# Performance work log

Hardware: AMD Instinct MI355X
Metric: run time of the kernel (lower is better)

Reference implementation:

```python
import jax, jax.numpy as jnp
import numpy as np

B, L, C, W, NH, FS = 8, 8, 64, 32, 128, 5
PAD = FS // 2
LN_EPS = 1e-5


def _conv(x, w, b, pad):
    y = jax.lax.conv_general_dilated(x, w, (1, 1), [(pad, pad), (pad, pad)],
                                     dimension_numbers=('NCHW', 'OIHW', 'NCHW'))
    return y + b[None, :, None, None]


def _stem(x, w1, b1, lnw, lnb, w2, b2):
    # conv(fs) -> LayerNorm over [C,W,W] -> ReLU -> conv(1x1)
    y = _conv(x, w1, b1, PAD)
    mu = jnp.mean(y, axis=(1, 2, 3), keepdims=True)
    var = jnp.var(y, axis=(1, 2, 3), keepdims=True)
    y = (y - mu) * jax.lax.rsqrt(var + LN_EPS) * lnw[None] + lnb[None]
    return _conv(jax.nn.relu(y), w2, b2, 0)


def setup_inputs() -> dict:
    key = jax.random.key(0)
    ks = jax.random.split(key, 8)
    f = lambda k, shp: jax.random.normal(k, shp, jnp.float32) * 0.02
    return {
        'in_query': jax.random.normal(ks[0], (B, C, W, W), jnp.float32),
        'in_keys': jax.random.normal(ks[1], (B, L, C, W, W), jnp.float32),
        'in_values': jax.random.normal(ks[2], (B, L, C, W, W), jnp.float32),
        's_w1': f(ks[3], (C, C, FS, FS)), 's_b1': jnp.zeros((C,), jnp.float32),
        's_lnw': jnp.ones((C, W, W), jnp.float32), 's_lnb': jnp.zeros((C, W, W), jnp.float32),
        's_w2': f(ks[4], (NH, C, 1, 1)), 's_b2': jnp.zeros((NH,), jnp.float32),
        'c_w1': f(ks[5], (C, C, FS, FS)), 'c_b1': jnp.zeros((C,), jnp.float32),
        'c_lnw': jnp.ones((C, W, W), jnp.float32), 'c_lnb': jnp.zeros((C, W, W), jnp.float32),
        'c_w2': f(ks[6], (NH, C, 1, 1)), 'c_b2': jnp.zeros((NH,), jnp.float32),
    }


def reference(in_query, in_keys, in_values,
              s_w1, s_b1, s_lnw, s_lnb, s_w2, s_b2,
              c_w1, c_b1, c_lnw, c_lnb, c_w2, c_b2):
    b, c, w, h = in_query.shape
    l = in_keys.shape[1]
    # ---- spatial attention: tokens = pixels, features = channels ----
    qf = in_query.reshape(b, c, w * h).transpose(0, 2, 1)            # [B, WH, C]
    kf = in_keys.transpose(0, 1, 3, 4, 2).reshape(b, l * w * h, c)   # [B, LWH, C]
    vf = in_values.transpose(0, 1, 3, 4, 2).reshape(b, l * w * h, c)
    a_sp = jax.nn.softmax(jnp.einsum('bnc,bmc->bnm', qf, kf), axis=-1)  # [B, WH, LWH]
    sp = jnp.einsum('bnm,bmc->bnc', a_sp, vf).reshape(b, w, h, c).transpose(0, 3, 1, 2)
    # ---- channel attention: tokens = channels, features = pixels ----
    qc = in_query.reshape(b, c, w * h)                               # [B, C, WH]
    kc = in_keys.reshape(b, l * c, h * w)                            # [B, LC, WH]
    vc = in_values.reshape(b, l * c, h * w)
    a_ch = jax.nn.softmax(jnp.einsum('bcn,bmn->bcm', qc, kc), axis=-1)  # [B, C, LC]
    ch = jnp.einsum('bcm,bmn->bcn', a_ch, vc).reshape(b, c, w, h)
    # ---- conv-LN-ReLU-conv stems on residual-added branches ----
    s_attn = _stem(sp + in_query, s_w1, s_b1, s_lnw, s_lnb, s_w2, s_b2)
    c_attn = _stem(ch + in_query, c_w1, c_b1, c_lnw, c_lnb, c_w2, c_b2)
    return (s_attn, c_attn)
```

## Files before the change

### kernel.cpp

```cpp
#include <hip/hip_runtime.h>


#define LOG2E 1.44269504088896340736f

typedef __attribute__((ext_vector_type(8))) short short8;
typedef __attribute__((ext_vector_type(4))) float f4;

#define MFMA16(a, b, c) __builtin_amdgcn_mfma_f32_16x16x32_bf16(a, b, c, 0, 0, 0)

#define GLOAD_LDS16(gp, lp) __builtin_amdgcn_global_load_lds( \
    (const __attribute__((address_space(1))) void*)(gp), \
    (__attribute__((address_space(3))) void*)(lp), 16, 0, 0)

__device__ __forceinline__ unsigned short f2bf(float f) {
  union { float f; unsigned u; } v; v.f = f;
  unsigned r = v.u + 0x7FFFu + ((v.u >> 16) & 1u);
  return (unsigned short)(r >> 16);
}
__device__ __forceinline__ unsigned short f2bf_rz(float f) {
  union { float f; unsigned u; } v; v.f = f;
  return (unsigned short)(v.u >> 16);
}
__device__ __forceinline__ float bf2f(unsigned short h) {
  union { unsigned u; float f; } v; v.u = ((unsigned)h) << 16;
  return v.f;
}
__device__ __forceinline__ float exp2fast(float x) {
#if __has_builtin(__builtin_amdgcn_exp2f)
  return __builtin_amdgcn_exp2f(x);
#else
  return exp2f(x);
#endif
}

#define O_STATS 0ul
#define O_W1T   256ul
#define O_W2B   409856ul
#define O_LNW   442624ul
#define O_LNB   704768ul
#define O_QT    966912ul
#define O_KSP   2015488ul
#define O_VT    10404096ul
#define O_NUM   18792704ul
#define O_DEN   35569920ul
#define O_SP    36094208ul
#define O_PCH   40288512ul
#define O_XS    40812800ul
#define O_XC    41861376ul
#define O_YT    42909952ul

__global__ __launch_bounds__(256) void k1_prep(
    const float* __restrict__ q, const float* __restrict__ keys,
    const float* __restrict__ values,
    const float* __restrict__ sw1, const float* __restrict__ slnw,
    const float* __restrict__ slnb, const float* __restrict__ sw2,
    const float* __restrict__ cw1, const float* __restrict__ clnw,
    const float* __restrict__ clnb, const float* __restrict__ cw2,
    char* __restrict__ ws)
{
  __shared__ __align__(16) unsigned char SM1[49152];
  const int t = threadIdx.x;

  if (blockIdx.x < 128) {
    float* Sp = (float*)(ws + O_SP);
    const int bid = blockIdx.x;
    if (bid == 0 && t < 64) ((float*)(ws + O_STATS))[t] = 0.f;
    const int b = bid >> 4, colT = (bid >> 2) & 3, kt = bid & 3;
    const int w = t >> 6, lane = t & 63;
    const int low4 = lane & 15, quad = lane >> 4;
    const int dl = lane >> 1, dh = lane & 1;
    const int k00 = kt * 256;

    f4 acc[4][2];
#pragma unroll
    for (int m = 0; m < 4; ++m)
#pragma unroll
      for (int n = 0; n < 2; ++n) acc[m][n] = (f4){0.f, 0.f, 0.f, 0.f};

    auto stageAll = [&](int bo, int k0) {
#pragma unroll
      for (int gi = 0; gi < 4; ++gi) {
        const int g = w + gi * 4;
        const int n = g >> 1, sub = g & 1;
        const int l = sub * 32 + dl;
        const float* gp = keys + (size_t)(b * 512 + colT * 128 + n * 16 + (l & 15)) * 1024
                          + k0 + (l >> 4) * 8 + dh * 4;
        GLOAD_LDS16(gp, SM1 + bo + (size_t)(n * 128 + sub * 64) * 16);
      }
#pragma unroll
      for (int gi = 0; gi < 2; ++gi) {
        const int g = w + gi * 4;
        const int m = g >> 1, sub = g & 1;
        const int l = sub * 32 + dl;
        const float* gp = q + (size_t)(b * 64 + m * 16 + (l & 15)) * 1024
                          + k0 + (l >> 4) * 8 + dh * 4;
        GLOAD_LDS16(gp, SM1 + bo + 16384 + (size_t)(m * 128 + sub * 64) * 16);
      }
    };

    stageAll(0, k00);
    for (int it = 0; it < 8; ++it) {
      const int bo = (it & 1) * 24576;
      const char* cb = (const char*)SM1 + bo;
      __syncthreads();
      if (it < 7) stageAll(bo ^ 24576, k00 + (it + 1) * 32);

      short8 ah[4], al[4];
#pragma unroll
      for (int m = 0; m < 4; ++m) {
        const float* fp = (const float*)(cb + 16384 + (size_t)(m * 128 + lane * 2) * 16);
        float4 u0 = ((const float4*)fp)[0];
        float4 u1 = ((const float4*)fp)[1];
        float vv[8] = {u0.x, u0.y, u0.z, u0.w, u1.x, u1.y, u1.z, u1.w};
#pragma unroll
        for (int j = 0; j < 8; ++j) {
          float sv = vv[j] * LOG2E;
          unsigned short hi = f2bf(sv);
          ah[m][j] = (short)hi;
          al[m][j] = (short)f2bf(sv - bf2f(hi));
        }
      }
#pragma unroll
      for (int n2 = 0; n2 < 2; ++n2) {
        const int n = w * 2 + n2;
        const float* fp = (const float*)(cb + (size_t)(n * 128 + lane * 2) * 16);
        float4 u0 = ((const float4*)fp)[0];
        float4 u1 = ((const float4*)fp)[1];
        float vv[8] = {u0.x, u0.y, u0.z, u0.w, u1.x, u1.y, u1.z, u1.w};
        short8 bh, bl;
#pragma unroll
        for (int j = 0; j < 8; ++j) {
          unsigned short hi = f2bf(vv[j]);
          bh[j] = (short)hi;
          bl[j] = (short)f2bf(vv[j] - bf2f(hi));
        }
#pragma unroll
        for (int m = 0; m < 4; ++m) {
          acc[m][n2] = MFMA16(ah[m], bh, acc[m][n2]);
          acc[m][n2] = MFMA16(al[m], bh, acc[m][n2]);
          acc[m][n2] = MFMA16(ah[m], bl, acc[m][n2]);
        }
      }
    }

#pragma unroll
    for (int m = 0; m < 4; ++m)
#pragma unroll
      for (int n2 = 0; n2 < 2; ++n2)
#pragma unroll
        for (int r = 0; r < 4; ++r) {
          const int row = m * 16 + quad * 4 + r;
          const int col = colT * 128 + (w * 2 + n2) * 16 + low4;
          Sp[(((size_t)kt * 8 + b) * 64 + row) * 512 + col] = acc[m][n2][r];
        }
    return;
  }

  float (*T)[65] = (float(*)[65])SM1;
  const int job = blockIdx.x - 128;

  if (job < 2240) {
    int kind, mat = 0, sel = 0;
    if (job < 1024)      { kind = 0; mat = job >> 4; }
    else if (job < 2048) { kind = 1; mat = (job - 1024) >> 4; }
    else if (job < 2176) { kind = 2; mat = (job - 2048) >> 4; }
    else                 { kind = 3; sel = (job - 2176) >> 4; }
    const int pt = job & 15, p0 = pt * 64;
    const float* src =
        kind == 0 ? keys : kind == 1 ? values : kind == 2 ? q
        : (sel == 0 ? slnw : sel == 1 ? slnb : sel == 2 ? clnw : clnb);
    src += (size_t)mat * 65536;

    const int r0 = t >> 4, c4 = (t & 15) * 4;
    if (kind == 1) {
      unsigned short* VTp = (unsigned short*)(ws + O_VT);
      const int b = mat >> 3, l = mat & 7;
#pragma unroll
      for (int pass = 0; pass < 4; ++pass) {
        const int r = pass * 16 + r0;
        float4 v = *(const float4*)(src + (size_t)r * 1024 + p0 + c4);
        ushort4 o;
        o.x = f2bf(v.x); o.y = f2bf(v.y); o.z = f2bf(v.z); o.w = f2bf(v.w);
        *(ushort4*)(VTp + ((size_t)b * 64 + r) * 8192 + l * 1024 + p0 + c4) = o;
      }
      return;
    }
#pragma unroll
    for (int pass = 0; pass < 4; ++pass) {
      const int r = pass * 16 + r0;
      float4 v = *(const float4*)(src + (size_t)r * 1024 + p0 + c4);
      T[r][c4] = v.x; T[r][c4 + 1] = v.y; T[r][c4 + 2] = v.z; T[r][c4 + 3] = v.w;
    }
    __syncthreads();
#pragma unroll
    for (int pass = 0; pass < 2; ++pass) {
      const int p = pass * 32 + (t >> 3), cs = (t & 7) * 8;
      short8 o;
      if (kind == 0) {
#pragma unroll
        for (int j = 0; j < 8; ++j) o[j] = (short)f2bf(T[cs + j][p] * LOG2E);
        const int b = mat >> 3, l = mat & 7;
        *(short8*)((unsigned short*)(ws + O_KSP) +
                   ((size_t)b * 8192 + l * 1024 + p0 + p) * 64 + cs) = o;
      } else if (kind == 2) {
#pragma unroll
        for (int j = 0; j < 8; ++j) o[j] = (short)f2bf(T[cs + j][p]);
        *(short8*)((unsigned short*)(ws + O_QT) +
                   ((size_t)mat * 1024 + p0 + p) * 64 + cs) = o;
      } else {
#pragma unroll
        for (int j = 0; j < 8; ++j) o[j] = (short)f2bf(T[cs + j][p]);
        unsigned long off = (sel & 1) ? O_LNB : O_LNW;
        *(short8*)((unsigned short*)(ws + off) +
                   ((size_t)(sel >> 1) * 1024 + p0 + p) * 64 + cs) = o;
      }
    }
    return;
  }

  {
    unsigned i = (job - 2240) * 256u + t;
    if (i < 204800u) {
      unsigned ci = i & 63u, co = (i >> 6) & 63u, tt = i >> 12;
      unsigned off = tt % 25u, st = tt / 25u;
      const float* w = st ? cw1 : sw1;
      ((unsigned short*)(ws + O_W1T))[i] = f2bf(w[(co * 64u + ci) * 25u + off]);
      return;
    }
    i -= 204800u;
    if (i < 16384u) {
      unsigned c = i & 63u, nh = (i >> 6) & 127u, st = i >> 13;
      const float* w = st ? cw2 : sw2;
      ((unsigned short*)(ws + O_W2B))[i] = f2bf(w[nh * 64u + c]);
    }
  }
}

__global__ __launch_bounds__(256) void k2_soft_spat(char* __restrict__ ws)
{
  __shared__ __align__(16) unsigned char SM[49152];

  if (blockIdx.x < 32) {
    const float* Sp = (const float*)(ws + O_SP);
    unsigned short* P = (unsigned short*)(ws + O_PCH);
    const int bid = blockIdx.x;
    const int b = bid >> 2, rt = bid & 3;
    const int row = rt * 16 + (threadIdx.x >> 4), tc = threadIdx.x & 15;

    float sv[32];
    float mx = -1e30f;
#pragma unroll
    for (int jj = 0; jj < 32; ++jj) {
      const int col = jj * 16 + tc;
      size_t base = ((size_t)b * 64 + row) * 512 + col;
      float v = Sp[base] + Sp[base + 262144] + Sp[base + 524288] + Sp[base + 786432];
      sv[jj] = v;
      mx = fmaxf(mx, v);
    }
#pragma unroll
    for (int o = 1; o < 16; o <<= 1) mx = fmaxf(mx, __shfl_xor(mx, o, 64));
    float sum = 0.f;
#pragma unroll
    for (int jj = 0; jj < 32; ++jj) {
      float e = exp2fast(sv[jj] - mx);
      sv[jj] = e;
      sum += e;
    }
#pragma unroll
    for (int o = 1; o < 16; o <<= 1) sum += __shfl_xor(sum, o, 64);
    const float rs = 1.0f / sum;
#pragma unroll
    for (int jj = 0; jj < 32; ++jj)
      P[((size_t)b * 64 + row) * 512 + jj * 16 + tc] = f2bf(sv[jj] * rs);
    return;
  }

  unsigned short (*Kt)[4096] = (unsigned short(*)[4096])(SM);
  unsigned short (*Vt)[4096] = (unsigned short(*)[4096])(SM + 16384);
  unsigned short (*Pl)[2048] = (unsigned short(*)[2048])(SM + 32768);

  const unsigned short* QT = (const unsigned short*)(ws + O_QT);
  const unsigned short* KSP = (const unsigned short*)(ws + O_KSP);
  const unsigned short* VTg = (const unsigned short*)(ws + O_VT);
  unsigned short* NUM = (unsigned short*)(ws + O_NUM);
  float* DEN = (float*)(ws + O_DEN);

  const int bid = blockIdx.x - 32;
  const int b = bid >> 6;
  const int qt = (bid >> 3) & 7;
  const int s = bid & 7;
  const int t = threadIdx.x;
  const int w = t >> 6, lane = t & 63;
  const int low4 = lane & 15, quad = lane >> 4;

  const unsigned short* KSPb = KSP + (size_t)b * 8192 * 64;
  const unsigned short* VTb = VTg + (size_t)b * 64 * 8192;
  const int qbase = qt * 128 + w * 32;
  const int kvbase = s * 1024;

  int cn[2], cks[2], cqd[2], cl4[2];
#pragma unroll
  for (int pass = 0; pass < 2; ++pass) {
    const int c = pass * 256 + t;
    cn[pass] = c >> 7; cks[pass] = (c >> 6) & 1;
    cqd[pass] = (c >> 4) & 3; cl4[pass] = c & 15;
  }

  short8 qa[2][2];
#pragma unroll
  for (int mi = 0; mi < 2; ++mi)
#pragma unroll
    for (int ks = 0; ks < 2; ++ks)
      qa[mi][ks] = *(const short8*)(QT +
          ((size_t)(b * 1024 + qbase + mi * 16 + low4)) * 64 + ks * 32 + quad * 8);

  short8 vones;
#pragma unroll
  for (int j = 0; j < 8; ++j) vones[j] = (short)0x3F80;

  f4 accO[2][4], accD[2];
#pragma unroll
  for (int m = 0; m < 2; ++m) {
    accD[m] = (f4){0.f, 0.f, 0.f, 0.f};
#pragma unroll
    for (int n = 0; n < 4; ++n) accO[m][n] = (f4){0.f, 0.f, 0.f, 0.f};
  }

#pragma unroll
  for (int pass = 0; pass < 2; ++pass) {
    GLOAD_LDS16(KSPb + ((size_t)(kvbase + cn[pass] * 16 + cl4[pass])) * 64 +
                    cks[pass] * 32 + cqd[pass] * 8,
                &Kt[0][(pass * 256 + w * 64) * 8]);
    GLOAD_LDS16(VTb + ((size_t)(cn[pass] * 16 + cl4[pass])) * 8192 + kvbase +
                    cks[pass] * 32 + cqd[pass] * 8,
                &Vt[0][(pass * 256 + w * 64) * 8]);
  }

  const int pswz = ((low4 >> 2) & 3) << 1;
  for (int it = 0; it < 16; ++it) {
    const int d = it & 1;
    __syncthreads();
    if (it < 15) {
      const int kv1 = kvbase + (it + 1) * 64;
#pragma unroll
      for (int pass = 0; pass < 2; ++pass) {
        GLOAD_LDS16(KSPb + ((size_t)(kv1 + cn[pass] * 16 + cl4[pass])) * 64 +
                        cks[pass] * 32 + cqd[pass] * 8,
                    &Kt[d ^ 1][(pass * 256 + w * 64) * 8]);
        GLOAD_LDS16(VTb + ((size_t)(cn[pass] * 16 + cl4[pass])) * 8192 + kv1 +
                        cks[pass] * 32 + cqd[pass] * 8,
                    &Vt[d ^ 1][(pass * 256 + w * 64) * 8]);
      }
    }
#pragma unroll
    for (int n = 0; n < 4; ++n) {
      f4 sS[2];
#pragma unroll
      for (int mi = 0; mi < 2; ++mi) sS[mi] = (f4){0.f, 0.f, 0.f, 0.f};
#pragma unroll
      for (int ks = 0; ks < 2; ++ks) {
        short8 kb = *(const short8*)&Kt[d][((n * 2 + ks) * 64 + lane) * 8];
#pragma unroll
        for (int mi = 0; mi < 2; ++mi) sS[mi] = MFMA16(qa[mi][ks], kb, sS[mi]);
      }
      const int cpr = (((n * 2 + (low4 >> 3)) ^ (quad << 1)) << 3) + (low4 & 7);
#pragma unroll
      for (int mi = 0; mi < 2; ++mi) {
        unsigned short* pw = &Pl[w][(mi * 16 + quad * 4) * 64 + cpr];
#pragma unroll
        for (int r = 0; r < 4; ++r)
          pw[r * 64] = f2bf_rz(exp2fast(sS[mi][r]));
      }
    }
#pragma unroll
    for (int ks = 0; ks < 2; ++ks) {
      short8 vb[4];
#pragma unroll
      for (int n2 = 0; n2 < 4; ++n2)
        vb[n2] = *(const short8*)&Vt[d][((n2 * 2 + ks) * 64 + lane) * 8];
      const int cr = (((ks * 4 + quad) ^ pswz) << 3);
#pragma unroll
      for (int m = 0; m < 2; ++m) {
        short8 pa = *(const short8*)&Pl[w][(m * 16 + low4) * 64 + cr];
        accD[m] = MFMA16(pa, vones, accD[m]);
#pragma unroll
        for (int n2 = 0; n2 < 4; ++n2) accO[m][n2] = MFMA16(pa, vb[n2], accO[m][n2]);
      }
    }
  }

#pragma unroll
  for (int m = 0; m < 2; ++m)
#pragma unroll
    for (int r = 0; r < 4; ++r) {
      const int row = qbase + m * 16 + quad * 4 + r;
      const size_t base = ((size_t)(b * 1024 + row) * 8 + s);
#pragma unroll
      for (int n2 = 0; n2 < 4; ++n2)
        NUM[base * 64 + n2 * 16 + low4] = f2bf(accO[m][n2][r]);
      if (low4 == 0) DEN[base] = accD[m][r];
    }
}

__global__ __launch_bounds__(256) void k3_chanB_fin(
    const float* __restrict__ values, char* __restrict__ ws)
{
  if (blockIdx.x < 128) {
    const unsigned short* P = (const unsigned short*)(ws + O_PCH);
    const unsigned short* QT = (const unsigned short*)(ws + O_QT);
    unsigned short* Xc = (unsigned short*)(ws + O_XC);

    const int bid = blockIdx.x;
    const int b = bid >> 4, pt = bid & 15;
    const int w = threadIdx.x >> 6, lane = threadIdx.x & 63;
    const int low4 = lane & 15, quad = lane >> 4;
    const int p = pt * 64 + w * 16 + low4;

    f4 acc[4];
#pragma unroll
    for (int m = 0; m < 4; ++m) acc[m] = (f4){0.f, 0.f, 0.f, 0.f};

    const float* vbase = values + (size_t)b * 524288 + p;
    for (int ks = 0; ks < 16; ++ks) {
      short8 vbv;
      const float* vp = vbase + (size_t)(ks * 32 + quad * 8) * 1024;
#pragma unroll
      for (int j = 0; j < 8; ++j) vbv[j] = (short)f2bf(vp[(size_t)j * 1024]);
#pragma unroll
      for (int m = 0; m < 4; ++m) {
        short8 a = *(const short8*)(P + ((size_t)(b * 64 + m * 16 + low4)) * 512 + ks * 32 + quad * 8);
        acc[m] = MFMA16(a, vbv, acc[m]);
      }
    }
#pragma unroll
    for (int m = 0; m < 4; ++m)
#pragma unroll
      for (int r = 0; r < 4; ++r) {
        const int c = m * 16 + quad * 4 + r;
        size_t o = ((size_t)(b * 1024 + p)) * 64 + c;
        Xc[o] = f2bf(acc[m][r] + bf2f(QT[o]));
      }
    return;
  }

  {
    const unsigned short* NUM = (const unsigned short*)(ws + O_NUM);
    const float* DEN = (const float*)(ws + O_DEN);
    const unsigned short* QT = (const unsigned short*)(ws + O_QT);
    unsigned short* Xs = (unsigned short*)(ws + O_XS);

    const unsigned i = (blockIdx.x - 128) * 256u + threadIdx.x;
    const int c0 = (i & 15) * 4;
    const unsigned row = i >> 4;

    float dtot = 0.f;
#pragma unroll
    for (int sq = 0; sq < 2; ++sq) {
      float4 dv = *(const float4*)(DEN + (size_t)row * 8 + sq * 4);
      dtot += dv.x + dv.y + dv.z + dv.w;
    }
    float n4[4] = {0.f, 0.f, 0.f, 0.f};
#pragma unroll
    for (int s = 0; s < 8; ++s) {
      ushort4 pv = *(const ushort4*)(NUM + ((size_t)row * 8 + s) * 64 + c0);
      n4[0] += bf2f(pv.x); n4[1] += bf2f(pv.y);
      n4[2] += bf2f(pv.z); n4[3] += bf2f(pv.w);
    }
    const float rd = 1.0f / dtot;
    size_t ob = (size_t)row * 64 + c0;
    ushort4 qv = *(const ushort4*)(QT + ob);
    ushort4 o4;
    o4.x = f2bf(n4[0] * rd + bf2f(qv.x));
    o4.y = f2bf(n4[1] * rd + bf2f(qv.y));
    o4.z = f2bf(n4[2] * rd + bf2f(qv.z));
    o4.w = f2bf(n4[3] * rd + bf2f(qv.w));
    *(ushort4*)(Xs + ob) = o4;
  }
}

__device__ __forceinline__ void conv5_body(char* ws, const float* b1p, int s, int bid)
{
  __shared__ float Hbuf[2][16][65];
  __shared__ float red[2][2];

  const int b = bid >> 5, pt = bid & 31;
  const int w = threadIdx.x >> 6, lane = threadIdx.x & 63;
  const int low4 = lane & 15, quad = lane >> 4;
  const int wsub = w & 1, half = w >> 1;

  const unsigned short* X = (const unsigned short*)(ws + (s ? O_XC : O_XS));
  const unsigned short* W1t = (const unsigned short*)(ws + O_W1T);
  unsigned short* Yt = (unsigned short*)(ws + O_YT);
  float* stats = (float*)(ws + O_STATS);

  const int p = pt * 32 + wsub * 16 + low4;
  const int y0 = p >> 5, x0 = p & 31;

  f4 acc[4];
#pragma unroll
  for (int m = 0; m < 4; ++m) acc[m] = (f4){0.f, 0.f, 0.f, 0.f};

  const int o0 = half ? 13 : 0, o1 = half ? 25 : 13;
  for (int off = o0; off < o1; ++off) {
    const int dy = off / 5 - 2, dx = off % 5 - 2;
    const int ys = y0 + dy, xs = x0 + dx;
    const bool valid = ((unsigned)ys < 32u) & ((unsigned)xs < 32u);
    const int psrc = valid ? (p + dy * 32 + dx) : p;
    const unsigned short* xp = X + ((size_t)(b * 1024 + psrc)) * 64;
    const unsigned short* wp = W1t + ((size_t)((s * 25 + off) * 64)) * 64;
#pragma unroll
    for (int ks = 0; ks < 2; ++ks) {
      short8 bv = *(const short8*)(xp + ks * 32 + quad * 8);
      if (!valid) bv = (short8)0;
#pragma unroll
      for (int m = 0; m < 4; ++m) {
        short8 av = *(const short8*)(wp + (m * 16 + low4) * 64 + ks * 32 + quad * 8);
        acc[m] = MFMA16(av, bv, acc[m]);
      }
    }
  }

  if (half) {
#pragma unroll
    for (int m = 0; m < 4; ++m)
#pragma unroll
      for (int r = 0; r < 4; ++r)
        Hbuf[wsub][low4][m * 16 + quad * 4 + r] = acc[m][r];
  }
  __syncthreads();
  if (!half) {
    float ls = 0.f, ls2 = 0.f;
#pragma unroll
    for (int m = 0; m < 4; ++m)
#pragma unroll
      for (int r = 0; r < 4; ++r) {
        const int co = m * 16 + quad * 4 + r;
        float y = acc[m][r] + Hbuf[wsub][low4][co] + b1p[co];
        Yt[((size_t)((s * 8 + b) * 1024 + p)) * 64 + co] = f2bf(y);
        ls += y; ls2 += y * y;
      }
#pragma unroll
    for (int o = 1; o < 64; o <<= 1) {
      ls += __shfl_xor(ls, o, 64);
      ls2 += __shfl_xor(ls2, o, 64);
    }
    if (lane == 0) { red[0][wsub] = ls; red[1][wsub] = ls2; }
  }
  __syncthreads();
  if (threadIdx.x == 0) {
    atomicAdd(&stats[(s * 8 + b) * 2 + 0], red[0][0] + red[0][1]);
    atomicAdd(&stats[(s * 8 + b) * 2 + 1], red[1][0] + red[1][1]);
  }
}

__device__ __forceinline__ void final_body(char* ws, const float* b2p,
                                           float* out, int s, int bid)
{
  const int b = bid >> 5, pt = bid & 31;
  const int w = threadIdx.x >> 6, lane = threadIdx.x & 63;
  const int low4 = lane & 15, quad = lane >> 4;
  const int p2 = pt * 32 + (w & 1) * 16 + low4;
  const int nh0 = (w >> 1) * 64;

  const unsigned short* Yt = (const unsigned short*)(ws + O_YT);
  const unsigned short* LNW = (const unsigned short*)(ws + O_LNW);
  const unsigned short* LNB = (const unsigned short*)(ws + O_LNB);
  const unsigned short* W2b = (const unsigned short*)(ws + O_W2B);
  const float* stats = (const float*)(ws + O_STATS);

  const float inv = 1.0f / 65536.0f;
  const float mu = stats[(s * 8 + b) * 2 + 0] * inv;
  const float ms = stats[(s * 8 + b) * 2 + 1] * inv;
  const float rsig = rsqrtf(ms - mu * mu + 1e-5f);

  f4 acc[4];
#pragma unroll
  for (int m = 0; m < 4; ++m) acc[m] = (f4){0.f, 0.f, 0.f, 0.f};

#pragma unroll
  for (int ks = 0; ks < 2; ++ks) {
    size_t yo = ((size_t)((s * 8 + b) * 1024 + p2)) * 64 + ks * 32 + quad * 8;
    size_t lo = ((size_t)(s * 1024 + p2)) * 64 + ks * 32 + quad * 8;
    short8 yv = *(const short8*)(Yt + yo);
    short8 lw8 = *(const short8*)(LNW + lo);
    short8 lb8 = *(const short8*)(LNB + lo);
    short8 zv;
#pragma unroll
    for (int j = 0; j < 8; ++j) {
      float z = (bf2f((unsigned short)yv[j]) - mu) * rsig * bf2f((unsigned short)lw8[j]) +
                bf2f((unsigned short)lb8[j]);
      zv[j] = (short)f2bf(fmaxf(z, 0.f));
    }
#pragma unroll
    for (int m = 0; m < 4; ++m) {
      short8 a = *(const short8*)(W2b + ((size_t)(s * 128 + nh0 + m * 16 + low4)) * 64 + ks * 32 + quad * 8);
      acc[m] = MFMA16(a, zv, acc[m]);
    }
  }
#pragma unroll
  for (int m = 0; m < 4; ++m)
#pragma unroll
    for (int r = 0; r < 4; ++r) {
      const int nh = nh0 + m * 16 + quad * 4 + r;
      out[((size_t)((s * 8 + b) * 128 + nh)) * 1024 + p2] = acc[m][r] + b2p[nh];
    }
}

__global__ __launch_bounds__(256) void k4_conv5(
    char* __restrict__ ws, const float* __restrict__ sb1,
    const float* __restrict__ cb1)
{
  if (blockIdx.x < 256) conv5_body(ws, sb1, 0, blockIdx.x);
  else                  conv5_body(ws, cb1, 1, blockIdx.x - 256);
}

__global__ __launch_bounds__(256) void k5_final(
    char* __restrict__ ws, const float* __restrict__ sb2,
    const float* __restrict__ cb2, float* __restrict__ out)
{
  if (blockIdx.x < 256) final_body(ws, sb2, out, 0, blockIdx.x);
  else                  final_body(ws, cb2, out, 1, blockIdx.x - 256);
}

extern "C" void kernel_launch(void* const* d_in, const int* in_sizes, int n_in,
                              void* d_out, int out_size, void* d_ws, size_t ws_size,
                              hipStream_t stream)
{
  const float* q    = (const float*)d_in[0];
  const float* keys = (const float*)d_in[1];
  const float* vals = (const float*)d_in[2];
  const float* sw1  = (const float*)d_in[3];
  const float* sb1  = (const float*)d_in[4];
  const float* slnw = (const float*)d_in[5];
  const float* slnb = (const float*)d_in[6];
  const float* sw2  = (const float*)d_in[7];
  const float* sb2  = (const float*)d_in[8];
  const float* cw1  = (const float*)d_in[9];
  const float* cb1  = (const float*)d_in[10];
  const float* clnw = (const float*)d_in[11];
  const float* clnb = (const float*)d_in[12];
  const float* cw2  = (const float*)d_in[13];
  const float* cb2  = (const float*)d_in[14];
  char* ws = (char*)d_ws;

  k1_prep<<<3232, 256, 0, stream>>>(q, keys, vals, sw1, slnw, slnb, sw2,
                                    cw1, clnw, clnb, cw2, ws);
  k2_soft_spat<<<544, 256, 0, stream>>>(ws);
  k3_chanB_fin<<<640, 256, 0, stream>>>(vals, ws);
  k4_conv5<<<512, 256, 0, stream>>>(ws, sb1, cb1);
  k5_final<<<512, 256, 0, stream>>>(ws, sb2, cb2, (float*)d_out);
}
```

Before: 201.8 us.

## Fuse five kernels into one persistent kernel with global atomic barriers

Replaces the five separate launches with a single 512-block persistent kernel whose phases are separated by software grid barriers built on agent-scope atomics. Work from stages that used to be separate kernels is reassigned across the fixed block count, for example chanB alongside stem conv5 and final alongside the second conv5. The aim is to remove launch gaps and tail effects between kernels. In exchange it depends on all 512 blocks being co-resident (launch_bounds 256,2 plus 48KB LDS), adds spin-wait barrier cost, and runs early phases with fewer blocks, which reduces parallelism.

```diff
diff --git a/kernel.cpp b/kernel.cpp
--- a/kernel.cpp
+++ b/kernel.cpp
@@ -2,6 +2,7 @@
 
 
 #define LOG2E 1.44269504088896340736f
+#define NBLK 512u
 
 typedef __attribute__((ext_vector_type(8))) short short8;
 typedef __attribute__((ext_vector_type(4))) float f4;
@@ -34,6 +35,7 @@
 }
 
 #define O_STATS 0ul
+#define O_BAR   192ul
 #define O_W1T   256ul
 #define O_W2B   409856ul
 #define O_LNW   442624ul
@@ -49,115 +51,128 @@
 #define O_XC    41861376ul
 #define O_YT    42909952ul
 
-__global__ __launch_bounds__(256) void k1_prep(
+__device__ __forceinline__ void gbar(unsigned* __restrict__ bar, int idx)
+{
+  __syncthreads();
+  if (threadIdx.x == 0) {
+    __threadfence();
+    __hip_atomic_fetch_add(&bar[idx], 1u, __ATOMIC_RELEASE,
+                           __HIP_MEMORY_SCOPE_AGENT);
+    while (__hip_atomic_load(&bar[idx], __ATOMIC_ACQUIRE,
+                             __HIP_MEMORY_SCOPE_AGENT) < NBLK)
+      __builtin_amdgcn_s_sleep(2);
+    __threadfence();
+  }
+  __syncthreads();
+}
+
+__device__ __forceinline__ void chanS_body(
+    const float* __restrict__ q, const float* __restrict__ keys,
+    char* __restrict__ ws, int bid, unsigned char* SM1)
+{
+  const int t = threadIdx.x;
+  float* Sp = (float*)(ws + O_SP);
+  const int b = bid >> 4, colT = (bid >> 2) & 3, kt = bid & 3;
+  const int w = t >> 6, lane = t & 63;
+  const int low4 = lane & 15, quad = lane >> 4;
+  const int dl = lane >> 1, dh = lane & 1;
+  const int k00 = kt * 256;
+
+  f4 acc[4][2];
+#pragma unroll
+  for (int m = 0; m < 4; ++m)
+#pragma unroll
+    for (int n = 0; n < 2; ++n) acc[m][n] = (f4){0.f, 0.f, 0.f, 0.f};
+
+  auto stageAll = [&](int bo, int k0) {
+#pragma unroll
+    for (int gi = 0; gi < 4; ++gi) {
+      const int g = w + gi * 4;
+      const int n = g >> 1, sub = g & 1;
+      const int l = sub * 32 + dl;
+      const float* gp = keys + (size_t)(b * 512 + colT * 128 + n * 16 + (l & 15)) * 1024
+                        + k0 + (l >> 4) * 8 + dh * 4;
+      GLOAD_LDS16(gp, SM1 + bo + (size_t)(n * 128 + sub * 64) * 16);
+    }
+#pragma unroll
+    for (int gi = 0; gi < 2; ++gi) {
+      const int g = w + gi * 4;
+      const int m = g >> 1, sub = g & 1;
+      const int l = sub * 32 + dl;
+      const float* gp = q + (size_t)(b * 64 + m * 16 + (l & 15)) * 1024
+                        + k0 + (l >> 4) * 8 + dh * 4;
+      GLOAD_LDS16(gp, SM1 + bo + 16384 + (size_t)(m * 128 + sub * 64) * 16);
+    }
+  };
+
+  stageAll(0, k00);
+  for (int it = 0; it < 8; ++it) {
+    const int bo = (it & 1) * 24576;
+    const char* cb = (const char*)SM1 + bo;
+    __syncthreads();
+    if (it < 7) stageAll(bo ^ 24576, k00 + (it + 1) * 32);
+
+    short8 ah[4], al[4];
+#pragma unroll
+    for (int m = 0; m < 4; ++m) {
+      const float* fp = (const float*)(cb + 16384 + (size_t)(m * 128 + lane * 2) * 16);
+      float4 u0 = ((const float4*)fp)[0];
+      float4 u1 = ((const float4*)fp)[1];
+      float vv[8] = {u0.x, u0.y, u0.z, u0.w, u1.x, u1.y, u1.z, u1.w};
+#pragma unroll
+      for (int j = 0; j < 8; ++j) {
+        float sv = vv[j] * LOG2E;
+        unsigned short hi = f2bf(sv);
+        ah[m][j] = (short)hi;
+        al[m][j] = (short)f2bf(sv - bf2f(hi));
+      }
+    }
+#pragma unroll
+    for (int n2 = 0; n2 < 2; ++n2) {
+      const int n = w * 2 + n2;
+      const float* fp = (const float*)(cb + (size_t)(n * 128 + lane * 2) * 16);
+      float4 u0 = ((const float4*)fp)[0];
+      float4 u1 = ((const float4*)fp)[1];
+      float vv[8] = {u0.x, u0.y, u0.z, u0.w, u1.x, u1.y, u1.z, u1.w};
+      short8 bh, bl;
+#pragma unroll
+      for (int j = 0; j < 8; ++j) {
+        unsigned short hi = f2bf(vv[j]);
+        bh[j] = (short)hi;
+        bl[j] = (short)f2bf(vv[j] - bf2f(hi));
+      }
+#pragma unroll
+      for (int m = 0; m < 4; ++m) {
+        acc[m][n2] = MFMA16(ah[m], bh, acc[m][n2]);
+        acc[m][n2] = MFMA16(al[m], bh, acc[m][n2]);
+        acc[m][n2] = MFMA16(ah[m], bl, acc[m][n2]);
+      }
+    }
+  }
+
+#pragma unroll
+  for (int m = 0; m < 4; ++m)
+#pragma unroll
+    for (int n2 = 0; n2 < 2; ++n2)
+#pragma unroll
+      for (int r = 0; r < 4; ++r) {
+        const int row = m * 16 + quad * 4 + r;
+        const int col = colT * 128 + (w * 2 + n2) * 16 + low4;
+        Sp[(((size_t)kt * 8 + b) * 64 + row) * 512 + col] = acc[m][n2][r];
+      }
+}
+
+__device__ __forceinline__ void prep_job(
     const float* __restrict__ q, const float* __restrict__ keys,
     const float* __restrict__ values,
     const float* __restrict__ sw1, const float* __restrict__ slnw,
     const float* __restrict__ slnb, const float* __restrict__ sw2,
     const float* __restrict__ cw1, const float* __restrict__ clnw,
     const float* __restrict__ clnb, const float* __restrict__ cw2,
-    char* __restrict__ ws)
-{
-  __shared__ __align__(16) unsigned char SM1[49152];
+    char* __restrict__ ws, int job, unsigned char* SMraw)
+{
+  float (*T)[65] = (float(*)[65])SMraw;
   const int t = threadIdx.x;
-
-  if (blockIdx.x < 128) {
-    float* Sp = (float*)(ws + O_SP);
-    const int bid = blockIdx.x;
-    if (bid == 0 && t < 64) ((float*)(ws + O_STATS))[t] = 0.f;
-    const int b = bid >> 4, colT = (bid >> 2) & 3, kt = bid & 3;
-    const int w = t >> 6, lane = t & 63;
-    const int low4 = lane & 15, quad = lane >> 4;
-    const int dl = lane >> 1, dh = lane & 1;
-    const int k00 = kt * 256;
-
-    f4 acc[4][2];
-#pragma unroll
-    for (int m = 0; m < 4; ++m)
-#pragma unroll
-      for (int n = 0; n < 2; ++n) acc[m][n] = (f4){0.f, 0.f, 0.f, 0.f};
-
-    auto stageAll = [&](int bo, int k0) {
-#pragma unroll
-      for (int gi = 0; gi < 4; ++gi) {
-        const int g = w + gi * 4;
-        const int n = g >> 1, sub = g & 1;
-        const int l = sub * 32 + dl;
-        const float* gp = keys + (size_t)(b * 512 + colT * 128 + n * 16 + (l & 15)) * 1024
-                          + k0 + (l >> 4) * 8 + dh * 4;
-        GLOAD_LDS16(gp, SM1 + bo + (size_t)(n * 128 + sub * 64) * 16);
-      }
-#pragma unroll
-      for (int gi = 0; gi < 2; ++gi) {
-        const int g = w + gi * 4;
-        const int m = g >> 1, sub = g & 1;
-        const int l = sub * 32 + dl;
-        const float* gp = q + (size_t)(b * 64 + m * 16 + (l & 15)) * 1024
-                          + k0 + (l >> 4) * 8 + dh * 4;
-        GLOAD_LDS16(gp, SM1 + bo + 16384 + (size_t)(m * 128 + sub * 64) * 16);
-      }
-    };
-
-    stageAll(0, k00);
-    for (int it = 0; it < 8; ++it) {
-      const int bo = (it & 1) * 24576;
-      const char* cb = (const char*)SM1 + bo;
-      __syncthreads();
-      if (it < 7) stageAll(bo ^ 24576, k00 + (it + 1) * 32);
-
-      short8 ah[4], al[4];
-#pragma unroll
-      for (int m = 0; m < 4; ++m) {
-        const float* fp = (const float*)(cb + 16384 + (size_t)(m * 128 + lane * 2) * 16);
-        float4 u0 = ((const float4*)fp)[0];
-        float4 u1 = ((const float4*)fp)[1];
-        float vv[8] = {u0.x, u0.y, u0.z, u0.w, u1.x, u1.y, u1.z, u1.w};
-#pragma unroll
-        for (int j = 0; j < 8; ++j) {
-          float sv = vv[j] * LOG2E;
-          unsigned short hi = f2bf(sv);
-          ah[m][j] = (short)hi;
-          al[m][j] = (short)f2bf(sv - bf2f(hi));
-        }
-      }
-#pragma unroll
-      for (int n2 = 0; n2 < 2; ++n2) {
-        const int n = w * 2 + n2;
-        const float* fp = (const float*)(cb + (size_t)(n * 128 + lane * 2) * 16);
-        float4 u0 = ((const float4*)fp)[0];
-        float4 u1 = ((const float4*)fp)[1];
-        float vv[8] = {u0.x, u0.y, u0.z, u0.w, u1.x, u1.y, u1.z, u1.w};
-        short8 bh, bl;
-#pragma unroll
-        for (int j = 0; j < 8; ++j) {
-          unsigned short hi = f2bf(vv[j]);
-          bh[j] = (short)hi;
-          bl[j] = (short)f2bf(vv[j] - bf2f(hi));
-        }
-#pragma unroll
-        for (int m = 0; m < 4; ++m) {
-          acc[m][n2] = MFMA16(ah[m], bh, acc[m][n2]);
-          acc[m][n2] = MFMA16(al[m], bh, acc[m][n2]);
-          acc[m][n2] = MFMA16(ah[m], bl, acc[m][n2]);
-        }
-      }
-    }
-
-#pragma unroll
-    for (int m = 0; m < 4; ++m)
-#pragma unroll
-      for (int n2 = 0; n2 < 2; ++n2)
-#pragma unroll
-        for (int r = 0; r < 4; ++r) {
-          const int row = m * 16 + quad * 4 + r;
-          const int col = colT * 128 + (w * 2 + n2) * 16 + low4;
-          Sp[(((size_t)kt * 8 + b) * 64 + row) * 512 + col] = acc[m][n2][r];
-        }
-    return;
-  }
-
-  float (*T)[65] = (float(*)[65])SM1;
-  const int job = blockIdx.x - 128;
 
   if (job < 2240) {
     int kind, mat = 0, sel = 0;
@@ -215,11 +230,12 @@
                    ((size_t)(sel >> 1) * 1024 + p0 + p) * 64 + cs) = o;
       }
     }
+    __syncthreads();
     return;
   }
 
   {
-    unsigned i = (job - 2240) * 256u + t;
+    unsigned i = (unsigned)(job - 2240) * 256u + t;
     if (i < 204800u) {
       unsigned ci = i & 63u, co = (i >> 6) & 63u, tt = i >> 12;
       unsigned off = tt % 25u, st = tt / 25u;
@@ -236,45 +252,43 @@
   }
 }
 
-__global__ __launch_bounds__(256) void k2_soft_spat(char* __restrict__ ws)
-{
-  __shared__ __align__(16) unsigned char SM[49152];
-
-  if (blockIdx.x < 32) {
-    const float* Sp = (const float*)(ws + O_SP);
-    unsigned short* P = (unsigned short*)(ws + O_PCH);
-    const int bid = blockIdx.x;
-    const int b = bid >> 2, rt = bid & 3;
-    const int row = rt * 16 + (threadIdx.x >> 4), tc = threadIdx.x & 15;
-
-    float sv[32];
-    float mx = -1e30f;
-#pragma unroll
-    for (int jj = 0; jj < 32; ++jj) {
-      const int col = jj * 16 + tc;
-      size_t base = ((size_t)b * 64 + row) * 512 + col;
-      float v = Sp[base] + Sp[base + 262144] + Sp[base + 524288] + Sp[base + 786432];
-      sv[jj] = v;
-      mx = fmaxf(mx, v);
-    }
-#pragma unroll
-    for (int o = 1; o < 16; o <<= 1) mx = fmaxf(mx, __shfl_xor(mx, o, 64));
-    float sum = 0.f;
-#pragma unroll
-    for (int jj = 0; jj < 32; ++jj) {
-      float e = exp2fast(sv[jj] - mx);
-      sv[jj] = e;
-      sum += e;
-    }
-#pragma unroll
-    for (int o = 1; o < 16; o <<= 1) sum += __shfl_xor(sum, o, 64);
-    const float rs = 1.0f / sum;
-#pragma unroll
-    for (int jj = 0; jj < 32; ++jj)
-      P[((size_t)b * 64 + row) * 512 + jj * 16 + tc] = f2bf(sv[jj] * rs);
-    return;
-  }
-
+__device__ __forceinline__ void soft_body(char* __restrict__ ws, int bid)
+{
+  const float* Sp = (const float*)(ws + O_SP);
+  unsigned short* P = (unsigned short*)(ws + O_PCH);
+  const int b = bid >> 2, rt = bid & 3;
+  const int row = rt * 16 + (threadIdx.x >> 4), tc = threadIdx.x & 15;
+
+  float sv[32];
+  float mx = -1e30f;
+#pragma unroll
+  for (int jj = 0; jj < 32; ++jj) {
+    const int col = jj * 16 + tc;
+    size_t base = ((size_t)b * 64 + row) * 512 + col;
+    float v = Sp[base] + Sp[base + 262144] + Sp[base + 524288] + Sp[base + 786432];
+    sv[jj] = v;
+    mx = fmaxf(mx, v);
+  }
+#pragma unroll
+  for (int o = 1; o < 16; o <<= 1) mx = fmaxf(mx, __shfl_xor(mx, o, 64));
+  float sum = 0.f;
+#pragma unroll
+  for (int jj = 0; jj < 32; ++jj) {
+    float e = exp2fast(sv[jj] - mx);
+    sv[jj] = e;
+    sum += e;
+  }
+#pragma unroll
+  for (int o = 1; o < 16; o <<= 1) sum += __shfl_xor(sum, o, 64);
+  const float rs = 1.0f / sum;
+#pragma unroll
+  for (int jj = 0; jj < 32; ++jj)
+    P[((size_t)b * 64 + row) * 512 + jj * 16 + tc] = f2bf(sv[jj] * rs);
+}
+
+__device__ __forceinline__ void spat_body(char* __restrict__ ws, int bid,
+                                          unsigned char* SM)
+{
   unsigned short (*Kt)[4096] = (unsigned short(*)[4096])(SM);
   unsigned short (*Vt)[4096] = (unsigned short(*)[4096])(SM + 16384);
   unsigned short (*Pl)[2048] = (unsigned short(*)[2048])(SM + 32768);
@@ -285,7 +299,6 @@
   unsigned short* NUM = (unsigned short*)(ws + O_NUM);
   float* DEN = (float*)(ws + O_DEN);
 
-  const int bid = blockIdx.x - 32;
   const int b = bid >> 6;
   const int qt = (bid >> 3) & 7;
   const int s = bid & 7;
@@ -402,80 +415,77 @@
     }
 }
 
-__global__ __launch_bounds__(256) void k3_chanB_fin(
-    const float* __restrict__ values, char* __restrict__ ws)
-{
-  if (blockIdx.x < 128) {
-    const unsigned short* P = (const unsigned short*)(ws + O_PCH);
-    const unsigned short* QT = (const unsigned short*)(ws + O_QT);
-    unsigned short* Xc = (unsigned short*)(ws + O_XC);
-
-    const int bid = blockIdx.x;
-    const int b = bid >> 4, pt = bid & 15;
-    const int w = threadIdx.x >> 6, lane = threadIdx.x & 63;
-    const int low4 = lane & 15, quad = lane >> 4;
-    const int p = pt * 64 + w * 16 + low4;
-
-    f4 acc[4];
-#pragma unroll
-    for (int m = 0; m < 4; ++m) acc[m] = (f4){0.f, 0.f, 0.f, 0.f};
-
-    const float* vbase = values + (size_t)b * 524288 + p;
-    for (int ks = 0; ks < 16; ++ks) {
-      short8 vbv;
-      const float* vp = vbase + (size_t)(ks * 32 + quad * 8) * 1024;
-#pragma unroll
-      for (int j = 0; j < 8; ++j) vbv[j] = (short)f2bf(vp[(size_t)j * 1024]);
-#pragma unroll
-      for (int m = 0; m < 4; ++m) {
-        short8 a = *(const short8*)(P + ((size_t)(b * 64 + m * 16 + low4)) * 512 + ks * 32 + quad * 8);
-        acc[m] = MFMA16(a, vbv, acc[m]);
-      }
-    }
-#pragma unroll
-    for (int m = 0; m < 4; ++m)
-#pragma unroll
-      for (int r = 0; r < 4; ++r) {
-        const int c = m * 16 + quad * 4 + r;
-        size_t o = ((size_t)(b * 1024 + p)) * 64 + c;
-        Xc[o] = f2bf(acc[m][r] + bf2f(QT[o]));
-      }
-    return;
-  }
-
-  {
-    const unsigned short* NUM = (const unsigned short*)(ws + O_NUM);
-    const float* DEN = (const float*)(ws + O_DEN);
-    const unsigned short* QT = (const unsigned short*)(ws + O_QT);
-    unsigned short* Xs = (unsigned short*)(ws + O_XS);
-
-    const unsigned i = (blockIdx.x - 128) * 256u + threadIdx.x;
-    const int c0 = (i & 15) * 4;
-    const unsigned row = i >> 4;
-
-    float dtot = 0.f;
-#pragma unroll
-    for (int sq = 0; sq < 2; ++sq) {
-      float4 dv = *(const float4*)(DEN + (size_t)row * 8 + sq * 4);
-      dtot += dv.x + dv.y + dv.z + dv.w;
-    }
-    float n4[4] = {0.f, 0.f, 0.f, 0.f};
-#pragma unroll
-    for (int s = 0; s < 8; ++s) {
-      ushort4 pv = *(const ushort4*)(NUM + ((size_t)row * 8 + s) * 64 + c0);
-      n4[0] += bf2f(pv.x); n4[1] += bf2f(pv.y);
-      n4[2] += bf2f(pv.z); n4[3] += bf2f(pv.w);
-    }
-    const float rd = 1.0f / dtot;
-    size_t ob = (size_t)row * 64 + c0;
-    ushort4 qv = *(const ushort4*)(QT + ob);
-    ushort4 o4;
-    o4.x = f2bf(n4[0] * rd + bf2f(qv.x));
-    o4.y = f2bf(n4[1] * rd + bf2f(qv.y));
-    o4.z = f2bf(n4[2] * rd + bf2f(qv.z));
-    o4.w = f2bf(n4[3] * rd + bf2f(qv.w));
-    *(ushort4*)(Xs + ob) = o4;
-  }
+__device__ __forceinline__ void fin_body(char* __restrict__ ws, int bid)
+{
+  const unsigned short* NUM = (const unsigned short*)(ws + O_NUM);
+  const float* DEN = (const float*)(ws + O_DEN);
+  const unsigned short* QT = (const unsigned short*)(ws + O_QT);
+  unsigned short* Xs = (unsigned short*)(ws + O_XS);
+
+  const unsigned i = (unsigned)bid * 256u + threadIdx.x;
+  const int c0 = (i & 15) * 4;
+  const unsigned row = i >> 4;
+
+  float dtot = 0.f;
+#pragma unroll
+  for (int sq = 0; sq < 2; ++sq) {
+    float4 dv = *(const float4*)(DEN + (size_t)row * 8 + sq * 4);
+    dtot += dv.x + dv.y + dv.z + dv.w;
+  }
+  float n4[4] = {0.f, 0.f, 0.f, 0.f};
+#pragma unroll
+  for (int s = 0; s < 8; ++s) {
+    ushort4 pv = *(const ushort4*)(NUM + ((size_t)row * 8 + s) * 64 + c0);
+    n4[0] += bf2f(pv.x); n4[1] += bf2f(pv.y);
+    n4[2] += bf2f(pv.z); n4[3] += bf2f(pv.w);
+  }
+  const float rd = 1.0f / dtot;
+  size_t ob = (size_t)row * 64 + c0;
+  ushort4 qv = *(const ushort4*)(QT + ob);
+  ushort4 o4;
+  o4.x = f2bf(n4[0] * rd + bf2f(qv.x));
+  o4.y = f2bf(n4[1] * rd + bf2f(qv.y));
+  o4.z = f2bf(n4[2] * rd + bf2f(qv.z));
+  o4.w = f2bf(n4[3] * rd + bf2f(qv.w));
+  *(ushort4*)(Xs + ob) = o4;
+}
+
+__device__ __forceinline__ void chanB_body(const float* __restrict__ values,
+                                           char* __restrict__ ws, int bid)
+{
+  const unsigned short* P = (const unsigned short*)(ws + O_PCH);
+  const unsigned short* QT = (const unsigned short*)(ws + O_QT);
+  unsigned short* Xc = (unsigned short*)(ws + O_XC);
+
+  const int b = bid >> 4, pt = bid & 15;
+  const int w = threadIdx.x >> 6, lane = threadIdx.x & 63;
+  const int low4 = lane & 15, quad = lane >> 4;
+  const int p = pt * 64 + w * 16 + low4;
+
+  f4 acc[4];
+#pragma unroll
+  for (int m = 0; m < 4; ++m) acc[m] = (f4){0.f, 0.f, 0.f, 0.f};
+
+  const float* vbase = values + (size_t)b * 524288 + p;
+  for (int ks = 0; ks < 16; ++ks) {
+    short8 vbv;
+    const float* vp = vbase + (size_t)(ks * 32 + quad * 8) * 1024;
+#pragma unroll
+    for (int j = 0; j < 8; ++j) vbv[j] = (short)f2bf(vp[(size_t)j * 1024]);
+#pragma unroll
+    for (int m = 0; m < 4; ++m) {
+      short8 a = *(const short8*)(P + ((size_t)(b * 64 + m * 16 + low4)) * 512 + ks * 32 + quad * 8);
+      acc[m] = MFMA16(a, vbv, acc[m]);
+    }
+  }
+#pragma unroll
+  for (int m = 0; m < 4; ++m)
+#pragma unroll
+    for (int r = 0; r < 4; ++r) {
+      const int c = m * 16 + quad * 4 + r;
+      size_t o = ((size_t)(b * 1024 + p)) * 64 + c;
+      Xc[o] = f2bf(acc[m][r] + bf2f(QT[o]));
+    }
 }
 
 __device__ __forceinline__ void conv5_body(char* ws, const float* b1p, int s, int bid)
@@ -551,6 +561,7 @@
     atomicAdd(&stats[(s * 8 + b) * 2 + 0], red[0][0] + red[0][1]);
     atomicAdd(&stats[(s * 8 + b) * 2 + 1], red[1][0] + red[1][1]);
   }
+  __syncthreads();
 }
 
 __device__ __forceinline__ void final_body(char* ws, const float* b2p,
@@ -606,20 +617,46 @@
     }
 }
 
-__global__ __launch_bounds__(256) void k4_conv5(
-    char* __restrict__ ws, const float* __restrict__ sb1,
-    const float* __restrict__ cb1)
-{
-  if (blockIdx.x < 256) conv5_body(ws, sb1, 0, blockIdx.x);
-  else                  conv5_body(ws, cb1, 1, blockIdx.x - 256);
-}
-
-__global__ __launch_bounds__(256) void k5_final(
-    char* __restrict__ ws, const float* __restrict__ sb2,
-    const float* __restrict__ cb2, float* __restrict__ out)
-{
-  if (blockIdx.x < 256) final_body(ws, sb2, out, 0, blockIdx.x);
-  else                  final_body(ws, cb2, out, 1, blockIdx.x - 256);
+__global__ __launch_bounds__(256, 2) void mega(
+    const float* __restrict__ q, const float* __restrict__ keys,
+    const float* __restrict__ values,
+    const float* __restrict__ sw1, const float* __restrict__ sb1,
+    const float* __restrict__ slnw, const float* __restrict__ slnb,
+    const float* __restrict__ sw2, const float* __restrict__ sb2,
+    const float* __restrict__ cw1, const float* __restrict__ cb1,
+    const float* __restrict__ clnw, const float* __restrict__ clnb,
+    const float* __restrict__ cw2, const float* __restrict__ cb2,
+    char* __restrict__ ws, float* __restrict__ out)
+{
+  __shared__ __align__(16) unsigned char SM[49152];
+  unsigned* bar = (unsigned*)(ws + O_BAR);
+  const int bid = blockIdx.x;
+
+  if (bid < 128) {
+    chanS_body(q, keys, ws, bid, SM);
+  } else {
+    for (int job = bid - 128; job < 3104; job += 384)
+      prep_job(q, keys, values, sw1, slnw, slnb, sw2, cw1, clnw, clnb, cw2,
+               ws, job, SM);
+  }
+  gbar(bar, 0);
+
+  spat_body(ws, bid, SM);
+  gbar(bar, 1);
+
+  if (bid < 32) soft_body(ws, bid);
+  fin_body(ws, bid);
+  gbar(bar, 2);
+
+  if (bid < 256)      conv5_body(ws, sb1, 0, bid);
+  else if (bid < 384) chanB_body(values, ws, bid - 256);
+  gbar(bar, 3);
+
+  if (bid < 256) conv5_body(ws, cb1, 1, bid);
+  else           final_body(ws, sb2, out, 0, bid - 256);
+  gbar(bar, 4);
+
+  if (bid < 256) final_body(ws, cb2, out, 1, bid);
 }
 
 extern "C" void kernel_launch(void* const* d_in, const int* in_sizes, int n_in,
@@ -643,10 +680,8 @@
   const float* cb2  = (const float*)d_in[14];
   char* ws = (char*)d_ws;
 
-  k1_prep<<<3232, 256, 0, stream>>>(q, keys, vals, sw1, slnw, slnb, sw2,
-                                    cw1, clnw, clnb, cw2, ws);
-  k2_soft_spat<<<544, 256, 0, stream>>>(ws);
-  k3_chanB_fin<<<640, 256, 0, stream>>>(vals, ws);
-  k4_conv5<<<512, 256, 0, stream>>>(ws, sb1, cb1);
-  k5_final<<<512, 256, 0, stream>>>(ws, sb2, cb2, (float*)d_out);
-}
+  (void)hipMemsetAsync(ws + O_STATS, 0, 256, stream);
+  mega<<<512, 256, 0, stream>>>(q, keys, vals, sw1, sb1, slnw, slnb, sw2, sb2,
+                                cw1, cb1, clnw, clnb, cw2, cb2,
+                                ws, (float*)d_out);
+}
```

New measurement: 718.7 us. 3.56x slower.
